# Performance work log

Measured on AMD Instinct MI355X. Metric: run time of the kernel, lower is better.

The kernel has to match this reference:

```python
import jax, jax.numpy as jnp
import numpy as np

IN_DIM, HIDDEN_DIM, OUT_DIM = 128, 128, 1
N_NODES, N_EDGES = 50000, 600000


def setup_inputs() -> dict:
    key = jax.random.key(0)
    k1, k2, k3, k4, k5, k6 = jax.random.split(key, 6)
    x = jax.random.normal(k1, (N_NODES, IN_DIM), dtype=jnp.float32)
    edge_index = jax.random.randint(k2, (2, N_EDGES), 0, N_NODES, dtype=jnp.int64)
    # Linear params (torch Linear: y = x @ W.T + b); store as [in, out] for einsum
    s1 = 1.0 / np.sqrt(2 * IN_DIM)
    W1 = jax.random.uniform(k3, (2 * IN_DIM, HIDDEN_DIM), jnp.float32, -s1, s1)
    b1 = jax.random.uniform(k4, (HIDDEN_DIM,), jnp.float32, -s1, s1)
    s2 = 1.0 / np.sqrt(HIDDEN_DIM)
    W2 = jax.random.uniform(k5, (HIDDEN_DIM, OUT_DIM), jnp.float32, -s2, s2)
    b2 = jax.random.uniform(k6, (OUT_DIM,), jnp.float32, -s2, s2)
    return {"x": x, "edge_index": edge_index, "W1": W1, "b1": b1, "W2": W2, "b2": b2}


def reference(x, edge_index, W1, b1, W2, b2):
    row, col = edge_index[0], edge_index[1]
    # gather endpoint features and concat -> [E, 2*in_dim]
    edge_input = jnp.concatenate([x[row], x[col]], axis=1)
    h = jax.nn.relu(edge_input @ W1 + b1)            # [E, hidden]
    return jax.nn.sigmoid(h @ W2 + b2)               # [E, out_dim]
```

## Files before the change

kernel.cpp:

```cpp
#include <hip/hip_runtime.h>
#include <hip/hip_bf16.h>
#include <math.h>

typedef __attribute__((ext_vector_type(8))) short short8;
typedef __attribute__((ext_vector_type(4))) float f32x4;

static __device__ __forceinline__ unsigned short f2bf(float f) {
    __hip_bfloat16 h = __float2bfloat16(f);
    return *reinterpret_cast<unsigned short*>(&h);
}

__global__ __launch_bounds__(256) void ep_prepw(
    const float* __restrict__ W1, unsigned short* __restrict__ W1s)
{
    const int gid = blockIdx.x * 256 + threadIdx.x;
    const int h   = gid >> 11;
    const int kb  = (gid >> 7) & 15;
    const int col = gid & 127;
    short8 v;
    #pragma unroll
    for (int j = 0; j < 8; ++j)
        v[j] = (short)f2bf(W1[(size_t)(h * 128 + kb * 8 + j) * 128 + col]);
    reinterpret_cast<short8*>(W1s)[gid] = v;
}

#define BM 128

__global__ __launch_bounds__(256) void ep_gemm(
    const float* __restrict__ x, const unsigned short* __restrict__ W1s,
    const float* __restrict__ b1,
    signed char* __restrict__ Aq, signed char* __restrict__ Bq,
    float* __restrict__ Ascale, float* __restrict__ Bscale,
    int nNodes, int nwg)
{
    __shared__ short8 xs[16 * BM];
    __shared__ short8 ws[16 * 128];

    const int tid = threadIdx.x;

    const int orig = blockIdx.x;
    const int q = nwg >> 3, r = nwg & 7;
    const int xcd = orig & 7, within = orig >> 3;
    const int base = (xcd < r) ? xcd * (q + 1) : r * (q + 1) + (xcd - r) * q;
    const int gi = base + within;

    const int Mblk  = gi >> 1;
    const int h     = gi & 1;
    const int node0 = Mblk * BM;
    signed char* __restrict__ outq = h ? Bq : Aq;
    float* __restrict__ outs = h ? Bscale : Ascale;

    #pragma unroll
    for (int i = 0; i < 8; ++i) {
        const int c = tid + i * 256;
        const int row = c >> 4, kb = c & 15;
        const int node = node0 + row;
        short8 v;
        if (node < nNodes) {
            const float4* src = reinterpret_cast<const float4*>(x + (size_t)node * 128 + kb * 8);
            const float4 p0 = src[0], p1 = src[1];
            v[0] = (short)f2bf(p0.x); v[1] = (short)f2bf(p0.y);
            v[2] = (short)f2bf(p0.z); v[3] = (short)f2bf(p0.w);
            v[4] = (short)f2bf(p1.x); v[5] = (short)f2bf(p1.y);
            v[6] = (short)f2bf(p1.z); v[7] = (short)f2bf(p1.w);
        } else {
            v = short8{0, 0, 0, 0, 0, 0, 0, 0};
        }
        xs[kb * BM + (row ^ kb)] = v;
    }
    #pragma unroll
    for (int i = 0; i < 8; ++i) {
        const int c = tid + i * 256;
        ws[c] = reinterpret_cast<const short8*>(W1s)[h * 2048 + c];
    }
    __syncthreads();

    const int w = tid >> 6, lane = tid & 63;
    const int wm = w * 32;
    const int lrow = lane & 15, lkb = lane >> 4;

    f32x4 acc[2][8];
    #pragma unroll
    for (int mt = 0; mt < 2; ++mt)
        #pragma unroll
        for (int nt = 0; nt < 8; ++nt)
            acc[mt][nt] = f32x4{0.f, 0.f, 0.f, 0.f};

    #pragma unroll
    for (int s = 0; s < 4; ++s) {
        const int kk = s * 4 + lkb;
        short8 af[2], bfr[8];
        #pragma unroll
        for (int mt = 0; mt < 2; ++mt)
            af[mt] = xs[kk * BM + ((wm + mt * 16 + lrow) ^ kk)];
        #pragma unroll
        for (int nt = 0; nt < 8; ++nt)
            bfr[nt] = ws[kk * 128 + nt * 16 + lrow];
        #pragma unroll
        for (int mt = 0; mt < 2; ++mt)
            #pragma unroll
            for (int nt = 0; nt < 8; ++nt)
                acc[mt][nt] = __builtin_amdgcn_mfma_f32_16x16x32_bf16(
                    af[mt], bfr[nt], acc[mt][nt], 0, 0, 0);
    }

    float b1v[8];
    #pragma unroll
    for (int nt = 0; nt < 8; ++nt)
        b1v[nt] = (h == 0) ? b1[nt * 16 + lrow] : 0.f;

    const int crow0 = (lane >> 4) * 4;
    #pragma unroll
    for (int mt = 0; mt < 2; ++mt) {
        #pragma unroll
        for (int r2 = 0; r2 < 4; ++r2) {
            float v[8];
            float m = 0.f;
            #pragma unroll
            for (int nt = 0; nt < 8; ++nt) {
                v[nt] = acc[mt][nt][r2] + b1v[nt];
                m = fmaxf(m, fabsf(v[nt]));
            }
            m = fmaxf(m, __shfl_xor(m, 1));
            m = fmaxf(m, __shfl_xor(m, 2));
            m = fmaxf(m, __shfl_xor(m, 4));
            m = fmaxf(m, __shfl_xor(m, 8));
            const float inv = 127.0f / fmaxf(m, 1e-30f);
            const int row = node0 + wm + mt * 16 + crow0 + r2;
            if (row < nNodes) {
                #pragma unroll
                for (int nt = 0; nt < 8; ++nt) {
                    const int qi = (int)rintf(v[nt] * inv);
                    outq[(size_t)row * 128 + nt * 16 + lrow] = (signed char)qi;
                }
                if (lrow == 0) outs[row] = m * (1.0f / 127.0f);
            }
        }
    }
}

__global__ __launch_bounds__(256) void ep_edges(
    const int* __restrict__ ei,
    const signed char* __restrict__ Aq, const signed char* __restrict__ Bq,
    const float* __restrict__ Ascale, const float* __restrict__ Bscale,
    const float* __restrict__ W2, const float* __restrict__ b2,
    float* __restrict__ out, int E)
{
    const int sub = threadIdx.x & 15;
    float w2f[8];
    #pragma unroll
    for (int j = 0; j < 8; ++j) w2f[j] = W2[sub * 8 + j];
    const float b2v = b2[0];

    const size_t stride = ((size_t)gridDim.x * blockDim.x) >> 4;
    for (size_t e = ((size_t)blockIdx.x * blockDim.x + threadIdx.x) >> 4;
         e < (size_t)E; e += stride) {
        const size_t r = (size_t)(unsigned)ei[e];
        const size_t c = (size_t)(unsigned)ei[E + e];

        const uint2 qa = *reinterpret_cast<const uint2*>(Aq + r * 128 + sub * 8);
        const uint2 qb = *reinterpret_cast<const uint2*>(Bq + c * 128 + sub * 8);
        const float sa = Ascale[r];
        const float sb = Bscale[c];

        float p = 0.f;
        #pragma unroll
        for (int j = 0; j < 8; ++j) {
            const unsigned ua = (j < 4) ? qa.x : qa.y;
            const unsigned ub = (j < 4) ? qb.x : qb.y;
            const int ia = (int)(signed char)(ua >> (8 * (j & 3)));
            const int ib = (int)(signed char)(ub >> (8 * (j & 3)));
            const float hv = fmaxf(fmaf((float)ia, sa, (float)ib * sb), 0.f);
            p = fmaf(hv, w2f[j], p);
        }

        p += __shfl_xor(p, 1);
        p += __shfl_xor(p, 2);
        p += __shfl_xor(p, 4);
        p += __shfl_xor(p, 8);

        if (sub == 0) out[e] = 1.f / (1.f + expf(-(p + b2v)));
    }
}

extern "C" void kernel_launch(void* const* d_in, const int* in_sizes, int n_in,
                              void* d_out, int out_size, void* d_ws, size_t ws_size,
                              hipStream_t stream) {
    const float* x  = (const float*)d_in[0];
    const int*   ei = (const int*)  d_in[1];
    const float* W1 = (const float*)d_in[2];
    const float* b1 = (const float*)d_in[3];
    const float* W2 = (const float*)d_in[4];
    const float* b2 = (const float*)d_in[5];
    float* out = (float*)d_out;

    const int nNodes = in_sizes[0] / 128;
    const int E      = in_sizes[1] / 2;

    unsigned short* W1s = (unsigned short*)d_ws;
    signed char* Aq     = (signed char*)(W1s + 2 * 2048 * 8);
    signed char* Bq     = Aq + (size_t)nNodes * 128;
    float* Ascale       = (float*)(Bq + (size_t)nNodes * 128);
    float* Bscale       = Ascale + nNodes;

    ep_prepw<<<16, 256, 0, stream>>>(W1, W1s);

    const int mblocks = (nNodes + BM - 1) / BM;
    const int nwg = mblocks * 2;
    ep_gemm<<<nwg, 256, 0, stream>>>(x, W1s, b1, Aq, Bq, Ascale, Bscale, nNodes, nwg);

    const int needed = (int)(((size_t)E * 16 + 255) / 256);
    const int edge_blocks = needed < 4096 ? needed : 4096;
    ep_edges<<<edge_blocks, 256, 0, stream>>>(ei, Aq, Bq, Ascale, Bscale, W2, b2, out, E);
}
```

Before: 55.95 us.

## Pre-swizzle W1 into MFMA fragment order, pack int8 stores, unroll edges by two

W1 is pre-laid-out in MFMA B-fragment order so each lane loads its fragment directly from global/L2 instead of staging W1 through LDS. The quantized hidden row is permuted so each lane writes 8 contiguous int8 bytes in one 64-bit store instead of 8 byte stores, and the W2 indexing is remapped to match. The edge kernel handles two edges per iteration to put more independent gathers in flight. The cost is repeated global weight reads per wave and higher register pressure in the edge loop.

```diff
diff --git a/kernel.cpp b/kernel.cpp
--- a/kernel.cpp
+++ b/kernel.cpp
@@ -11,30 +11,32 @@
 }
 
 __global__ __launch_bounds__(256) void ep_prepw(
-    const float* __restrict__ W1, unsigned short* __restrict__ W1s)
+    const float* __restrict__ W1, unsigned short* __restrict__ W1f)
 {
-    const int gid = blockIdx.x * 256 + threadIdx.x;
-    const int h   = gid >> 11;
-    const int kb  = (gid >> 7) & 15;
-    const int col = gid & 127;
+    const int gid  = blockIdx.x * 256 + threadIdx.x;
+    const int lane = gid & 63;
+    const int nt   = (gid >> 6) & 7;
+    const int s    = (gid >> 9) & 3;
+    const int h    = gid >> 11;
+    const int kk   = s * 4 + (lane >> 4);
+    const int col  = nt * 16 + (lane & 15);
     short8 v;
     #pragma unroll
     for (int j = 0; j < 8; ++j)
-        v[j] = (short)f2bf(W1[(size_t)(h * 128 + kb * 8 + j) * 128 + col]);
-    reinterpret_cast<short8*>(W1s)[gid] = v;
+        v[j] = (short)f2bf(W1[(size_t)(h * 128 + kk * 8 + j) * 128 + col]);
+    reinterpret_cast<short8*>(W1f)[gid] = v;
 }
 
 #define BM 128
 
 __global__ __launch_bounds__(256) void ep_gemm(
-    const float* __restrict__ x, const unsigned short* __restrict__ W1s,
+    const float* __restrict__ x, const unsigned short* __restrict__ W1f,
     const float* __restrict__ b1,
     signed char* __restrict__ Aq, signed char* __restrict__ Bq,
     float* __restrict__ Ascale, float* __restrict__ Bscale,
     int nNodes, int nwg)
 {
     __shared__ short8 xs[16 * BM];
-    __shared__ short8 ws[16 * 128];
 
     const int tid = threadIdx.x;
 
@@ -68,16 +70,12 @@
         }
         xs[kb * BM + (row ^ kb)] = v;
     }
-    #pragma unroll
-    for (int i = 0; i < 8; ++i) {
-        const int c = tid + i * 256;
-        ws[c] = reinterpret_cast<const short8*>(W1s)[h * 2048 + c];
-    }
     __syncthreads();
 
     const int w = tid >> 6, lane = tid & 63;
     const int wm = w * 32;
     const int lrow = lane & 15, lkb = lane >> 4;
+    const short8* __restrict__ Wf = reinterpret_cast<const short8*>(W1f) + (size_t)h * 2048;
 
     f32x4 acc[2][8];
     #pragma unroll
@@ -95,7 +93,7 @@
             af[mt] = xs[kk * BM + ((wm + mt * 16 + lrow) ^ kk)];
         #pragma unroll
         for (int nt = 0; nt < 8; ++nt)
-            bfr[nt] = ws[kk * 128 + nt * 16 + lrow];
+            bfr[nt] = Wf[(s * 8 + nt) * 64 + lane];
         #pragma unroll
         for (int mt = 0; mt < 2; ++mt)
             #pragma unroll
@@ -128,11 +126,15 @@
             const float inv = 127.0f / fmaxf(m, 1e-30f);
             const int row = node0 + wm + mt * 16 + crow0 + r2;
             if (row < nNodes) {
+                unsigned lo = 0, hi = 0;
                 #pragma unroll
-                for (int nt = 0; nt < 8; ++nt) {
-                    const int qi = (int)rintf(v[nt] * inv);
-                    outq[(size_t)row * 128 + nt * 16 + lrow] = (signed char)qi;
-                }
+                for (int nt = 0; nt < 4; ++nt)
+                    lo |= ((unsigned)(unsigned char)(signed char)(int)rintf(v[nt] * inv)) << (8 * nt);
+                #pragma unroll
+                for (int nt = 4; nt < 8; ++nt)
+                    hi |= ((unsigned)(unsigned char)(signed char)(int)rintf(v[nt] * inv)) << (8 * (nt - 4));
+                *reinterpret_cast<uint2*>(outq + (size_t)row * 128 + lrow * 8) =
+                    make_uint2(lo, hi);
                 if (lrow == 0) outs[row] = m * (1.0f / 127.0f);
             }
         }
@@ -149,37 +151,57 @@
     const int sub = threadIdx.x & 15;
     float w2f[8];
     #pragma unroll
-    for (int j = 0; j < 8; ++j) w2f[j] = W2[sub * 8 + j];
+    for (int j = 0; j < 8; ++j) w2f[j] = W2[j * 16 + sub];
     const float b2v = b2[0];
 
-    const size_t stride = ((size_t)gridDim.x * blockDim.x) >> 4;
-    for (size_t e = ((size_t)blockIdx.x * blockDim.x + threadIdx.x) >> 4;
-         e < (size_t)E; e += stride) {
-        const size_t r = (size_t)(unsigned)ei[e];
-        const size_t c = (size_t)(unsigned)ei[E + e];
-
-        const uint2 qa = *reinterpret_cast<const uint2*>(Aq + r * 128 + sub * 8);
-        const uint2 qb = *reinterpret_cast<const uint2*>(Bq + c * 128 + sub * 8);
-        const float sa = Ascale[r];
-        const float sb = Bscale[c];
-
-        float p = 0.f;
+    const size_t gsz = ((size_t)gridDim.x * blockDim.x) >> 4;
+    const size_t g0 = ((size_t)blockIdx.x * blockDim.x + threadIdx.x) >> 4;
+
+    for (size_t e = g0; e < (size_t)E; e += 2 * gsz) {
+        const size_t e2 = e + gsz;
+        const bool has2 = e2 < (size_t)E;
+
+        const size_t r1 = (size_t)(unsigned)ei[e];
+        const size_t c1 = (size_t)(unsigned)ei[E + e];
+        const uint2 qa1 = *reinterpret_cast<const uint2*>(Aq + r1 * 128 + sub * 8);
+        const uint2 qb1 = *reinterpret_cast<const uint2*>(Bq + c1 * 128 + sub * 8);
+        const float sa1 = Ascale[r1];
+        const float sb1 = Bscale[c1];
+
+        uint2 qa2 = make_uint2(0, 0), qb2 = make_uint2(0, 0);
+        float sa2 = 0.f, sb2 = 0.f;
+        if (has2) {
+            const size_t r2 = (size_t)(unsigned)ei[e2];
+            const size_t c2 = (size_t)(unsigned)ei[E + e2];
+            qa2 = *reinterpret_cast<const uint2*>(Aq + r2 * 128 + sub * 8);
+            qb2 = *reinterpret_cast<const uint2*>(Bq + c2 * 128 + sub * 8);
+            sa2 = Ascale[r2];
+            sb2 = Bscale[c2];
+        }
+
+        float p1 = 0.f, p2 = 0.f;
         #pragma unroll
         for (int j = 0; j < 8; ++j) {
-            const unsigned ua = (j < 4) ? qa.x : qa.y;
-            const unsigned ub = (j < 4) ? qb.x : qb.y;
-            const int ia = (int)(signed char)(ua >> (8 * (j & 3)));
-            const int ib = (int)(signed char)(ub >> (8 * (j & 3)));
-            const float hv = fmaxf(fmaf((float)ia, sa, (float)ib * sb), 0.f);
-            p = fmaf(hv, w2f[j], p);
-        }
-
-        p += __shfl_xor(p, 1);
-        p += __shfl_xor(p, 2);
-        p += __shfl_xor(p, 4);
-        p += __shfl_xor(p, 8);
-
-        if (sub == 0) out[e] = 1.f / (1.f + expf(-(p + b2v)));
+            const int sh = 8 * (j & 3);
+            const int ia1 = (int)(signed char)(((j < 4) ? qa1.x : qa1.y) >> sh);
+            const int ib1 = (int)(signed char)(((j < 4) ? qb1.x : qb1.y) >> sh);
+            const float h1 = fmaxf(fmaf((float)ia1, sa1, (float)ib1 * sb1), 0.f);
+            p1 = fmaf(h1, w2f[j], p1);
+            const int ia2 = (int)(signed char)(((j < 4) ? qa2.x : qa2.y) >> sh);
+            const int ib2 = (int)(signed char)(((j < 4) ? qb2.x : qb2.y) >> sh);
+            const float h2 = fmaxf(fmaf((float)ia2, sa2, (float)ib2 * sb2), 0.f);
+            p2 = fmaf(h2, w2f[j], p2);
+        }
+
+        p1 += __shfl_xor(p1, 1); p2 += __shfl_xor(p2, 1);
+        p1 += __shfl_xor(p1, 2); p2 += __shfl_xor(p2, 2);
+        p1 += __shfl_xor(p1, 4); p2 += __shfl_xor(p2, 4);
+        p1 += __shfl_xor(p1, 8); p2 += __shfl_xor(p2, 8);
+
+        if (sub == 0) {
+            out[e] = 1.f / (1.f + expf(-(p1 + b2v)));
+            if (has2) out[e2] = 1.f / (1.f + expf(-(p2 + b2v)));
+        }
     }
 }
 
@@ -197,17 +219,17 @@
     const int nNodes = in_sizes[0] / 128;
     const int E      = in_sizes[1] / 2;
 
-    unsigned short* W1s = (unsigned short*)d_ws;
-    signed char* Aq     = (signed char*)(W1s + 2 * 2048 * 8);
+    unsigned short* W1f = (unsigned short*)d_ws;
+    signed char* Aq     = (signed char*)(W1f + 4096 * 8);
     signed char* Bq     = Aq + (size_t)nNodes * 128;
     float* Ascale       = (float*)(Bq + (size_t)nNodes * 128);
     float* Bscale       = Ascale + nNodes;
 
-    ep_prepw<<<16, 256, 0, stream>>>(W1, W1s);
+    ep_prepw<<<16, 256, 0, stream>>>(W1, W1f);
 
     const int mblocks = (nNodes + BM - 1) / BM;
     const int nwg = mblocks * 2;
-    ep_gemm<<<nwg, 256, 0, stream>>>(x, W1s, b1, Aq, Bq, Ascale, Bscale, nNodes, nwg);
+    ep_gemm<<<nwg, 256, 0, stream>>>(x, W1f, b1, Aq, Bq, Ascale, Bscale, nNodes, nwg);
 
     const int needed = (int)(((size_t)E * 16 + 255) / 256);
     const int edge_blocks = needed < 4096 ? needed : 4096;
```

Measured after the change: 57.23 us. +2.3%, slower.

## Pack biased-uint8 hidden codes per lane, halve GEMM tile, use 8 lanes per edge

Applied to the files above, without the earlier changes.

The node GEMM tile shrinks from 128 to 64 rows, giving more workgroups. Each lane now packs its 8 quantized outputs into one 8-byte store instead of eight scattered byte stores. Values are stored as uint8 offset by 128, so unpacking needs no sign extension. The stored column order is permuted, and the edge kernel reorders W2 to match. The edge kernel uses 8 lanes per edge with 16-byte gathers and a shorter shuffle reduction, and runs a fixed grid of 2048 blocks.

```diff
diff --git a/kernel.cpp b/kernel.cpp
--- a/kernel.cpp
+++ b/kernel.cpp
@@ -8,6 +8,10 @@
 static __device__ __forceinline__ unsigned short f2bf(float f) {
     __hip_bfloat16 h = __float2bfloat16(f);
     return *reinterpret_cast<unsigned short*>(&h);
+}
+
+static __device__ __forceinline__ float ub2f(unsigned u, int b) {
+    return (float)((u >> (8 * b)) & 0xffu);
 }
 
 __global__ __launch_bounds__(256) void ep_prepw(
@@ -24,12 +28,12 @@
     reinterpret_cast<short8*>(W1s)[gid] = v;
 }
 
-#define BM 128
+#define BM 64
 
 __global__ __launch_bounds__(256) void ep_gemm(
     const float* __restrict__ x, const unsigned short* __restrict__ W1s,
     const float* __restrict__ b1,
-    signed char* __restrict__ Aq, signed char* __restrict__ Bq,
+    unsigned char* __restrict__ Aq, unsigned char* __restrict__ Bq,
     float* __restrict__ Ascale, float* __restrict__ Bscale,
     int nNodes, int nwg)
 {
@@ -47,11 +51,11 @@
     const int Mblk  = gi >> 1;
     const int h     = gi & 1;
     const int node0 = Mblk * BM;
-    signed char* __restrict__ outq = h ? Bq : Aq;
+    unsigned char* __restrict__ outq = h ? Bq : Aq;
     float* __restrict__ outs = h ? Bscale : Ascale;
 
     #pragma unroll
-    for (int i = 0; i < 8; ++i) {
+    for (int i = 0; i < 4; ++i) {
         const int c = tid + i * 256;
         const int row = c >> 4, kb = c & 15;
         const int node = node0 + row;
@@ -76,32 +80,24 @@
     __syncthreads();
 
     const int w = tid >> 6, lane = tid & 63;
-    const int wm = w * 32;
+    const int wm = w * 16;
     const int lrow = lane & 15, lkb = lane >> 4;
 
-    f32x4 acc[2][8];
-    #pragma unroll
-    for (int mt = 0; mt < 2; ++mt)
-        #pragma unroll
-        for (int nt = 0; nt < 8; ++nt)
-            acc[mt][nt] = f32x4{0.f, 0.f, 0.f, 0.f};
+    f32x4 acc[8];
+    #pragma unroll
+    for (int nt = 0; nt < 8; ++nt) acc[nt] = f32x4{0.f, 0.f, 0.f, 0.f};
 
     #pragma unroll
     for (int s = 0; s < 4; ++s) {
         const int kk = s * 4 + lkb;
-        short8 af[2], bfr[8];
-        #pragma unroll
-        for (int mt = 0; mt < 2; ++mt)
-            af[mt] = xs[kk * BM + ((wm + mt * 16 + lrow) ^ kk)];
+        const short8 af = xs[kk * BM + ((wm + lrow) ^ kk)];
+        short8 bfr[8];
         #pragma unroll
         for (int nt = 0; nt < 8; ++nt)
             bfr[nt] = ws[kk * 128 + nt * 16 + lrow];
         #pragma unroll
-        for (int mt = 0; mt < 2; ++mt)
-            #pragma unroll
-            for (int nt = 0; nt < 8; ++nt)
-                acc[mt][nt] = __builtin_amdgcn_mfma_f32_16x16x32_bf16(
-                    af[mt], bfr[nt], acc[mt][nt], 0, 0, 0);
+        for (int nt = 0; nt < 8; ++nt)
+            acc[nt] = __builtin_amdgcn_mfma_f32_16x16x32_bf16(af, bfr[nt], acc[nt], 0, 0, 0);
     }
 
     float b1v[8];
@@ -111,73 +107,77 @@
 
     const int crow0 = (lane >> 4) * 4;
     #pragma unroll
-    for (int mt = 0; mt < 2; ++mt) {
-        #pragma unroll
-        for (int r2 = 0; r2 < 4; ++r2) {
-            float v[8];
-            float m = 0.f;
+    for (int r2 = 0; r2 < 4; ++r2) {
+        float v[8];
+        float m = 0.f;
+        #pragma unroll
+        for (int nt = 0; nt < 8; ++nt) {
+            v[nt] = acc[nt][r2] + b1v[nt];
+            m = fmaxf(m, fabsf(v[nt]));
+        }
+        m = fmaxf(m, __shfl_xor(m, 1));
+        m = fmaxf(m, __shfl_xor(m, 2));
+        m = fmaxf(m, __shfl_xor(m, 4));
+        m = fmaxf(m, __shfl_xor(m, 8));
+        const float inv = 127.0f / fmaxf(m, 1e-30f);
+        const int row = node0 + wm + crow0 + r2;
+        if (row < nNodes) {
+            unsigned lo = 0, hi = 0;
             #pragma unroll
-            for (int nt = 0; nt < 8; ++nt) {
-                v[nt] = acc[mt][nt][r2] + b1v[nt];
-                m = fmaxf(m, fabsf(v[nt]));
-            }
-            m = fmaxf(m, __shfl_xor(m, 1));
-            m = fmaxf(m, __shfl_xor(m, 2));
-            m = fmaxf(m, __shfl_xor(m, 4));
-            m = fmaxf(m, __shfl_xor(m, 8));
-            const float inv = 127.0f / fmaxf(m, 1e-30f);
-            const int row = node0 + wm + mt * 16 + crow0 + r2;
-            if (row < nNodes) {
-                #pragma unroll
-                for (int nt = 0; nt < 8; ++nt) {
-                    const int qi = (int)rintf(v[nt] * inv);
-                    outq[(size_t)row * 128 + nt * 16 + lrow] = (signed char)qi;
-                }
-                if (lrow == 0) outs[row] = m * (1.0f / 127.0f);
-            }
+            for (int nt = 0; nt < 4; ++nt)
+                lo |= ((unsigned)(int)rintf(fmaf(v[nt], inv, 128.0f))) << (8 * nt);
+            #pragma unroll
+            for (int nt = 4; nt < 8; ++nt)
+                hi |= ((unsigned)(int)rintf(fmaf(v[nt], inv, 128.0f))) << (8 * (nt - 4));
+            *reinterpret_cast<uint2*>(outq + (size_t)row * 128 + lrow * 8) =
+                make_uint2(lo, hi);
+            if (lrow == 0) outs[row] = m * (1.0f / 127.0f);
         }
     }
 }
 
 __global__ __launch_bounds__(256) void ep_edges(
     const int* __restrict__ ei,
-    const signed char* __restrict__ Aq, const signed char* __restrict__ Bq,
+    const unsigned char* __restrict__ Aq, const unsigned char* __restrict__ Bq,
     const float* __restrict__ Ascale, const float* __restrict__ Bscale,
     const float* __restrict__ W2, const float* __restrict__ b2,
     float* __restrict__ out, int E)
 {
-    const int sub = threadIdx.x & 15;
-    float w2f[8];
-    #pragma unroll
-    for (int j = 0; j < 8; ++j) w2f[j] = W2[sub * 8 + j];
+    const int sub = threadIdx.x & 7;
+    float w2f[16];
+    #pragma unroll
+    for (int j = 0; j < 16; ++j)
+        w2f[j] = W2[(j & 7) * 16 + sub * 2 + (j >> 3)];
     const float b2v = b2[0];
 
-    const size_t stride = ((size_t)gridDim.x * blockDim.x) >> 4;
-    for (size_t e = ((size_t)blockIdx.x * blockDim.x + threadIdx.x) >> 4;
+    const size_t stride = ((size_t)gridDim.x * blockDim.x) >> 3;
+    for (size_t e = ((size_t)blockIdx.x * blockDim.x + threadIdx.x) >> 3;
          e < (size_t)E; e += stride) {
         const size_t r = (size_t)(unsigned)ei[e];
         const size_t c = (size_t)(unsigned)ei[E + e];
 
-        const uint2 qa = *reinterpret_cast<const uint2*>(Aq + r * 128 + sub * 8);
-        const uint2 qb = *reinterpret_cast<const uint2*>(Bq + c * 128 + sub * 8);
+        const uint4 qa = *reinterpret_cast<const uint4*>(Aq + r * 128 + sub * 16);
+        const uint4 qb = *reinterpret_cast<const uint4*>(Bq + c * 128 + sub * 16);
         const float sa = Ascale[r];
         const float sb = Bscale[c];
+        const float off = -128.0f * (sa + sb);
 
         float p = 0.f;
-        #pragma unroll
-        for (int j = 0; j < 8; ++j) {
-            const unsigned ua = (j < 4) ? qa.x : qa.y;
-            const unsigned ub = (j < 4) ? qb.x : qb.y;
-            const int ia = (int)(signed char)(ua >> (8 * (j & 3)));
-            const int ib = (int)(signed char)(ub >> (8 * (j & 3)));
-            const float hv = fmaxf(fmaf((float)ia, sa, (float)ib * sb), 0.f);
-            p = fmaf(hv, w2f[j], p);
+        const unsigned wa[4] = {qa.x, qa.y, qa.z, qa.w};
+        const unsigned wb[4] = {qb.x, qb.y, qb.z, qb.w};
+        #pragma unroll
+        for (int wd = 0; wd < 4; ++wd) {
+            #pragma unroll
+            for (int b = 0; b < 4; ++b) {
+                float t = fmaf(ub2f(wa[wd], b), sa, off);
+                t = fmaf(ub2f(wb[wd], b), sb, t);
+                p = fmaf(fmaxf(t, 0.f), w2f[wd * 4 + b], p);
+            }
         }
 
         p += __shfl_xor(p, 1);
         p += __shfl_xor(p, 2);
         p += __shfl_xor(p, 4);
-        p += __shfl_xor(p, 8);
 
         if (sub == 0) out[e] = 1.f / (1.f + expf(-(p + b2v)));
     }
@@ -198,8 +198,8 @@
     const int E      = in_sizes[1] / 2;
 
     unsigned short* W1s = (unsigned short*)d_ws;
-    signed char* Aq     = (signed char*)(W1s + 2 * 2048 * 8);
-    signed char* Bq     = Aq + (size_t)nNodes * 128;
+    unsigned char* Aq   = (unsigned char*)(W1s + 4096 * 8);
+    unsigned char* Bq   = Aq + (size_t)nNodes * 128;
     float* Ascale       = (float*)(Bq + (size_t)nNodes * 128);
     float* Bscale       = Ascale + nNodes;
 
@@ -209,7 +209,6 @@
     const int nwg = mblocks * 2;
     ep_gemm<<<nwg, 256, 0, stream>>>(x, W1s, b1, Aq, Bq, Ascale, Bscale, nNodes, nwg);
 
-    const int needed = (int)(((size_t)E * 16 + 255) / 256);
-    const int edge_blocks = needed < 4096 ? needed : 4096;
+    const int edge_blocks = 2048;
     ep_edges<<<edge_blocks, 256, 0, stream>>>(ei, Aq, Bq, Ascale, Bscale, W2, b2, out, E);
 }
```

Result: faster. 47.56 us (median of 2 runs) (-15.0%).
